# Performance work log

Hardware: AMD Instinct MI355X
Metric: run time of the kernel (lower is better)

## Reference

```python
import jax, jax.numpy as jnp
import numpy as np

N, K, D_IN, D_OUT = 50000, 16, 128, 256
C1, C2 = D_OUT // 4, D_OUT // 2  # 64, 128
E = N * K


def _lin(key, din, dout):
    return jax.random.normal(key, (din, dout), jnp.float32) * 0.02


def setup_inputs() -> dict:
    key = jax.random.key(0)
    ks = jax.random.split(key, 16)
    x = jax.random.normal(ks[0], (N, D_IN), jnp.float32)
    pos = jax.random.normal(ks[1], (N, 3), jnp.float32)
    normals = jax.random.normal(ks[2], (N, 3), jnp.float32)
    batch = jnp.zeros((N,), jnp.int32)
    # fixed k-regular graph standing in for knn_graph(pos, K); src != dst so
    # darboux's sqrt(|pos_j-pos_i|^2) is smooth everywhere
    dst = jnp.repeat(jnp.arange(N, dtype=jnp.int32), K)            # [E]
    off = jax.random.randint(ks[3], (E,), 1, N, jnp.int32)
    src = (dst + off) % N                                          # [E]
    edge_index = jnp.stack([src, dst])                             # [2,E]
    inp = dict(x=x, pos=pos, batch=batch, normals=normals, edge_index=edge_index)

    def add_mlp(name, k, din, dout):
        inp[name + '_w'] = _lin(k, din, dout)
        inp[name + '_b'] = jnp.zeros((dout,), jnp.float32)
        inp[name + '_g'] = jnp.ones((dout,), jnp.float32)
        inp[name + '_bt'] = jnp.zeros((dout,), jnp.float32)

    add_mlp('mlp1', ks[4], D_IN, D_OUT // 8)
    add_mlp('sc', ks[5], D_IN, D_OUT)
    add_mlp('mlp2', ks[6], C2, D_OUT)
    add_mlp('enc1', ks[7], 8, C1 // 2)
    inp['att1_w'] = _lin(ks[8], C1, C1)
    add_mlp('post1', ks[9], C1, C1)
    add_mlp('enc2', ks[10], 8, C2 // 2)
    inp['att2_w'] = _lin(ks[11], C2, C2)
    add_mlp('post2', ks[12], C2, C2)
    return inp


def _bn(h, g, bt, eps=1e-6):
    # BatchNorm1d, training-mode batch statistics (biased variance)
    m = h.mean(0)
    v = jnp.mean((h - m) ** 2, axis=0)
    return (h - m) * jax.lax.rsqrt(v + eps) * g + bt


def _lrelu(h):
    return jnp.where(h >= 0, h, 0.2 * h)


def _smlp(h, w, b, g, bt, act=True):
    # SharedMLP layer: Linear -> BN(eps=1e-6) -> LeakyReLU(0.2) (act optional)
    h = _bn(h @ w + b, g, bt)
    return _lrelu(h) if act else h


def _darboux(pi, pj, ni, nj):
    eps = 1e-10
    d = pj - pi                                            # [E,3]
    dot = lambda a, b: jnp.sum(a * b, axis=1, keepdims=True)
    nrm = lambda a: jnp.sqrt(jnp.sum(a * a, axis=1, keepdims=True))
    dist = nrm(d)
    lni, lnj = nrm(ni), nrm(nj)
    uq = jnp.cross(d, ni); vq = jnp.cross(uq, ni)
    uk = jnp.cross(d, nj); vk = jnp.cross(uk, nj)
    luq, lvq, luk, lvk = nrm(uq), nrm(vq), nrm(uk), nrm(vk)
    return jnp.concatenate([
        dist,
        dot(d, ni) / (dist * lni + eps),
        dot(d, nj) / (dist * lnj + eps),
        dot(ni, nj) / (lni * lnj + eps),
        dot(uq, uk) / (luq * luk + eps),
        dot(vq, vk) / (lvq * lvk + eps),
        dot(uq, vk) / (luq * lvk + eps),
        dot(vq, uk) / (lvq * luk + eps),
    ], axis=1)                                             # [E,8]


def _seg_softmax(h, idx, n):
    m = jax.ops.segment_max(h, idx, num_segments=n)        # [N,C]
    e = jnp.exp(h - m[idx])
    s = jax.ops.segment_sum(e, idx, num_segments=n)
    return e / (s[idx] + 1e-16)


def _lfa(src, dst, n, x, pos, normals, ew, eb, eg, ebt, aw, pw, pb, pg, pbt):
    rel = _darboux(pos[dst], pos[src], normals[dst], normals[src])  # [E,8]
    lse = _smlp(rel, ew, eb, eg, ebt)                               # [E,C/2]
    lf = jnp.concatenate([x[src], lse], axis=1)                     # [E,C]
    att = lf @ aw                                                   # [E,C]
    scores = _seg_softmax(att, dst, n)
    agg = jax.ops.segment_sum(scores * lf, dst, num_segments=n)     # [N,C]
    return _smlp(agg, pw, pb, pg, pbt)


def reference(x, pos, batch, normals, edge_index,
              mlp1_w, mlp1_b, mlp1_g, mlp1_bt,
              sc_w, sc_b, sc_g, sc_bt,
              mlp2_w, mlp2_b, mlp2_g, mlp2_bt,
              enc1_w, enc1_b, enc1_g, enc1_bt, att1_w,
              post1_w, post1_b, post1_g, post1_bt,
              enc2_w, enc2_b, enc2_g, enc2_bt, att2_w,
              post2_w, post2_b, post2_g, post2_bt):
    n = x.shape[0]
    src, dst = edge_index[0], edge_index[1]
    shortcut = _smlp(x, sc_w, sc_b, sc_g, sc_bt, act=False)         # [N,d_out]
    h = _smlp(x, mlp1_w, mlp1_b, mlp1_g, mlp1_bt)                   # [N,d_out//8]
    h = _lfa(src, dst, n, h, pos, normals,
             enc1_w, enc1_b, enc1_g, enc1_bt, att1_w,
             post1_w, post1_b, post1_g, post1_bt)                   # [N,d_out//4]
    h = _lfa(src, dst, n, h, pos, normals,
             enc2_w, enc2_b, enc2_g, enc2_bt, att2_w,
             post2_w, post2_b, post2_g, post2_bt)                   # [N,d_out//2]
    h = _smlp(h, mlp2_w, mlp2_b, mlp2_g, mlp2_bt, act=False)        # [N,d_out]
    return _lrelu(h + shortcut)
```

## Files before the change

kernel.cpp:

```cpp
#include <hip/hip_runtime.h>
#include <hip/hip_bf16.h>
#include <math.h>


typedef __attribute__((ext_vector_type(8))) short short8;
typedef __attribute__((ext_vector_type(4))) float floatx4;

#define NPART 16
#define PSTRIDE 4096

__device__ __forceinline__ float lrelu_f(float v) { return v >= 0.f ? v : 0.2f * v; }

__device__ __forceinline__ uint asu(float f) {
    union { float f; uint u; } c; c.f = f; return c.u;
}
__device__ __forceinline__ unsigned short f2bf(float f) {
    union { __hip_bfloat16 h; unsigned short u; } cv;
    cv.h = __float2bfloat16(f);
    return cv.u;
}
__device__ __forceinline__ unsigned short f2bf_r(float f) {
    return (unsigned short)((asu(f) + 0x8000u) >> 16);
}
__device__ __forceinline__ uint pack2bf_r(float lo, float hi) {
// ... 12 lines not shown
{
    int gid = blockIdx.x * 256 + threadIdx.x;
    int base = 0;
    for (int s = 0; s < 7; s++) {
        int c = pa.seg[s].cnt;
        if (gid < base + c) {
            int fi = gid - base;
            const float* w = pa.seg[s].src;
            const int Cout = pa.seg[s].Cout, KK = pa.seg[s].KK;
            const int l15 = fi & 15, g = (fi >> 4) & 3, rest = fi >> 6;
            const int kk = rest % KK, nt = rest / KK;
            const int col = nt * 16 + l15;
            short8 v;
#pragma unroll
            for (int e = 0; e < 8; e++)
                v[e] = (short)f2bf(w[(size_t)(kk * 32 + g * 8 + e) * Cout + col]);
            *reinterpret_cast<short8*>(pa.seg[s].dst + (size_t)fi * 8) = v;
            return;
        }
        base += c;
    }
}

template<bool AFF, bool IN16, bool MLP1>
__global__ __launch_bounds__(256)
void lin_mfma_kernel(const void* __restrict__ inv, const float* __restrict__ aff,
                     const short* __restrict__ wp, const float* __restrict__ b,
                     unsigned short* __restrict__ out16, double* __restrict__ st,
                     const short* __restrict__ wp1, const float* __restrict__ b1,
                     unsigned short* __restrict__ out1, double* __restrict__ st1, int n)
{
    __shared__ __align__(16) char aS[64 * 256];
    const int tid = threadIdx.x;
    const int w = tid >> 6, grp = (tid >> 4) & 3, l15 = tid & 15, lane = tid & 63;
    const int row0 = blockIdx.x * 64;
    const int poff = (blockIdx.x & (NPART - 1)) * PSTRIDE;
    double* stp = st + poff;
    {
        const int r = tid >> 2;
        const int p = tid & 3;
        const int chbase = p * 32;
        const int gr = row0 + r;
        if (gr < n) {
#pragma unroll
            for (int u = 0; u < 4; u++) {
                float h[8];
                if constexpr (IN16) {
                    const unsigned short* hrow = (const unsigned short*)inv + (size_t)gr * 128 + chbase + u * 8;
                    uint4 raw = *reinterpret_cast<const uint4*>(hrow);
                    h[0] = bf2f((unsigned short)(raw.x & 0xFFFF)); h[1] = bf2f((unsigned short)(raw.x >> 16));
                    h[2] = bf2f((unsigned short)(raw.y & 0xFFFF)); h[3] = bf2f((unsigned short)(raw.y >> 16));
                    h[4] = bf2f((unsigned short)(raw.z & 0xFFFF)); h[5] = bf2f((unsigned short)(raw.z >> 16));
                    h[6] = bf2f((unsigned short)(raw.w & 0xFFFF)); h[7] = bf2f((unsigned short)(raw.w >> 16));
                } else {
                    const float* hrow = (const float*)inv + (size_t)gr * 128 + chbase + u * 8;
                    float4 h0 = *reinterpret_cast<const float4*>(hrow);
                    float4 h1 = *reinterpret_cast<const float4*>(hrow + 4);
                    h[0] = h0.x; h[1] = h0.y; h[2] = h0.z; h[3] = h0.w;
                    h[4] = h1.x; h[5] = h1.y; h[6] = h1.z; h[7] = h1.w;
                }
                if constexpr (AFF) {
                    const float* ar = aff + chbase + u * 8;
                    const float* cr = aff + 128 + chbase + u * 8;
#pragma unroll
                    for (int i2 = 0; i2 < 8; i2++)
                        h[i2] = lrelu_f(fmaf(h[i2], ar[i2], cr[i2]));
                }
                uint4 pk;
                pk.x = pack2bf_r(h[0], h[1]); pk.y = pack2bf_r(h[2], h[3]);
                pk.z = pack2bf_r(h[4], h[5]); pk.w = pack2bf_r(h[6], h[7]);
                const int unit = (chbase >> 3) + u;
                *reinterpret_cast<uint4*>(aS + r * 256 + ((unit ^ (r & 7)) << 4)) = pk;
            }
        }
    }
    __syncthreads();

    short8 B[4][4]; float bias[4];
#pragma unroll
    for (int t = 0; t < 4; t++) {
        const int nt = w * 4 + t;
        bias[t] = b[nt * 16 + l15];
#pragma unroll
        for (int kk = 0; kk < 4; kk++)
            B[t][kk] = *reinterpret_cast<const short8*>(wp + (size_t)(((nt * 4 + kk) * 4 + grp) * 16 + l15) * 8);
    }
    float ssum[4] = {0.f, 0.f, 0.f, 0.f}, ssq[4] = {0.f, 0.f, 0.f, 0.f};
#pragma unroll
    for (int mt = 0; mt < 4; mt++) {
        short8 a[4];
        const int arow = mt * 16 + l15;
#pragma unroll
        for (int kk = 0; kk < 4; kk++)
            a[kk] = *reinterpret_cast<const short8*>(aS + arow * 256 + ((((kk << 2) + grp) ^ (arow & 7)) << 4));
#pragma unroll
        for (int t = 0; t < 4; t++) {
            floatx4 acc = {bias[t], bias[t], bias[t], bias[t]};
#pragma unroll
            for (int kk = 0; kk < 4; kk++)
                acc = __builtin_amdgcn_mfma_f32_16x16x32_bf16(a[kk], B[t][kk], acc, 0, 0, 0);
            const int c = (w * 4 + t) * 16 + l15;
#pragma unroll
            for (int r = 0; r < 4; r++) {
                const int grow = row0 + mt * 16 + grp * 4 + r;
                if (grow < n) {
                    out16[(size_t)grow * 256 + c] = f2bf_r(acc[r]);
                    ssum[t] += acc[r];
                    ssq[t] = fmaf(acc[r], acc[r], ssq[t]);
                }
            }
        }
    }
#pragma unroll
    for (int t = 0; t < 4; t++) {
        float s = ssum[t], q = ssq[t];
        s += __shfl_xor(s, 16); s += __shfl_xor(s, 32);
        q += __shfl_xor(q, 16); q += __shfl_xor(q, 32);
        if (lane < 16) {
            const int c = (w * 4 + t) * 16 + l15;
            atomicAdd(&stp[c], (double)s);
            atomicAdd(&stp[256 + c], (double)q);
        }
    }

    if constexpr (MLP1) {
        if (w < 2) {
            double* stp1 = st1 + poff;
            const float bias1 = b1[w * 16 + l15];
            short8 B1[4];
#pragma unroll
            for (int kk = 0; kk < 4; kk++)
                B1[kk] = *reinterpret_cast<const short8*>(wp1 + (size_t)(((w * 4 + kk) * 4 + grp) * 16 + l15) * 8);
            float s1 = 0.f, q1 = 0.f;
#pragma unroll
            for (int mt = 0; mt < 4; mt++) {
                short8 a[4];
                const int arow = mt * 16 + l15;
#pragma unroll
                for (int kk = 0; kk < 4; kk++)
                    a[kk] = *reinterpret_cast<const short8*>(aS + arow * 256 + ((((kk << 2) + grp) ^ (arow & 7)) << 4));
                floatx4 acc = {bias1, bias1, bias1, bias1};
#pragma unroll
                for (int kk = 0; kk < 4; kk++)
                    acc = __builtin_amdgcn_mfma_f32_16x16x32_bf16(a[kk], B1[kk], acc, 0, 0, 0);
                const int c = w * 16 + l15;
#pragma unroll
                for (int r = 0; r < 4; r++) {
                    const int grow = row0 + mt * 16 + grp * 4 + r;
                    if (grow < n) {
                        out1[(size_t)grow * 32 + c] = f2bf_r(acc[r]);
                        s1 += acc[r];
                        q1 = fmaf(acc[r], acc[r], q1);
                    }
                }
            }
            s1 += __shfl_xor(s1, 16); s1 += __shfl_xor(s1, 32);
            q1 += __shfl_xor(q1, 16); q1 += __shfl_xor(q1, 32);
            if (lane < 16) {
                const int c = w * 16 + l15;
                atomicAdd(&stp1[c], (double)s1);
                atomicAdd(&stp1[32 + c], (double)q1);
            }
        }
    }
}

__global__ __launch_bounds__(256)
void edge_enc_kernel(const int* __restrict__ src, const float* __restrict__ pos,
                     const float* __restrict__ nrm, unsigned short* __restrict__ rel16,
                     int E, double* __restrict__ stM)
{
    float s8[8] = {0, 0, 0, 0, 0, 0, 0, 0};
    float M[36];
#pragma unroll
    for (int k = 0; k < 36; k++) M[k] = 0.f;
    const int tid = threadIdx.x;

    for (int e = blockIdx.x * 256 + tid; e < E; e += gridDim.x * 256) {
        const int d = e >> 4;
        const int s = src[e];
        const float pix = pos[3 * d], piy = pos[3 * d + 1], piz = pos[3 * d + 2];
        const float pjx = pos[3 * s], pjy = pos[3 * s + 1], pjz = pos[3 * s + 2];
        const float nix = nrm[3 * d], niy = nrm[3 * d + 1], niz = nrm[3 * d + 2];
        const float njx = nrm[3 * s], njy = nrm[3 * s + 1], njz = nrm[3 * s + 2];
        const float dx = pjx - pix, dy = pjy - piy, dz = pjz - piz;
        const float dist = sqrtf(dx * dx + dy * dy + dz * dz);
        const float lni = sqrtf(nix * nix + niy * niy + niz * niz);
        const float lnj = sqrtf(njx * njx + njy * njy + njz * njz);
        const float uqx = dy * niz - dz * niy, uqy = dz * nix - dx * niz, uqz = dx * niy - dy * nix;
        const float vqx = uqy * niz - uqz * niy, vqy = uqz * nix - uqx * niz, vqz = uqx * niy - uqy * nix;
        const float ukx = dy * njz - dz * njy, uky = dz * njx - dx * njz, ukz = dx * njy - dy * njx;
        const float vkx = uky * njz - ukz * njy, vky = ukz * njx - ukx * njz, vkz = ukx * njy - uky * njx;
        const float luq = sqrtf(uqx * uqx + uqy * uqy + uqz * uqz);
        const float lvq = sqrtf(vqx * vqx + vqy * vqy + vqz * vqz);
        const float luk = sqrtf(ukx * ukx + uky * uky + ukz * ukz);
        const float lvk = sqrtf(vkx * vkx + vky * vky + vkz * vkz);
        const float eps = 1e-10f;
        float rv[8];
        rv[0] = dist;
        rv[1] = (dx * nix + dy * niy + dz * niz) / (dist * lni + eps);
        rv[2] = (dx * njx + dy * njy + dz * njz) / (dist * lnj + eps);
        rv[3] = (nix * njx + niy * njy + niz * njz) / (lni * lnj + eps);
        rv[4] = (uqx * ukx + uqy * uky + uqz * ukz) / (luq * luk + eps);
        rv[5] = (vqx * vkx + vqy * vky + vqz * vkz) / (lvq * lvk + eps);
        rv[6] = (uqx * vkx + uqy * vky + uqz * vkz) / (luq * lvk + eps);
        rv[7] = (vqx * ukx + vqy * uky + vqz * ukz) / (lvq * luk + eps);
        uint4 pk;
        pk.x = pack2bf_r(rv[0], rv[1]); pk.y = pack2bf_r(rv[2], rv[3]);
        pk.z = pack2bf_r(rv[4], rv[5]); pk.w = pack2bf_r(rv[6], rv[7]);
        *reinterpret_cast<uint4*>(rel16 + (size_t)e * 8) = pk;
#pragma unroll
        for (int i = 0; i < 8; i++) s8[i] += rv[i];
#pragma unroll
        for (int i = 0; i < 8; i++)
#pragma unroll
            for (int j = i; j < 8; j++)
                M[i * 8 - (i * (i - 1)) / 2 + (j - i)] = fmaf(rv[i], rv[j], M[i * 8 - (i * (i - 1)) / 2 + (j - i)]);
    }
#pragma unroll
    for (int k = 0; k < 8; k++) {
        float v = s8[k];
        v += __shfl_xor(v, 1); v += __shfl_xor(v, 2); v += __shfl_xor(v, 4);
        v += __shfl_xor(v, 8); v += __shfl_xor(v, 16); v += __shfl_xor(v, 32);
        s8[k] = v;
    }
#pragma unroll
    for (int k = 0; k < 36; k++) {
        float v = M[k];
        v += __shfl_xor(v, 1); v += __shfl_xor(v, 2); v += __shfl_xor(v, 4);
        v += __shfl_xor(v, 8); v += __shfl_xor(v, 16); v += __shfl_xor(v, 32);
        M[k] = v;
    }
    __shared__ float red[4][44];
    const int w = tid >> 6, lane = tid & 63;
    if (lane == 0) {
#pragma unroll
        for (int k = 0; k < 8; k++) red[w][k] = s8[k];
#pragma unroll
        for (int k = 0; k < 36; k++) red[w][8 + k] = M[k];
    }
    __syncthreads();
    if (tid < 44) {
        float tot = red[0][tid] + red[1][tid] + red[2][tid] + red[3][tid];
        atomicAdd(&stM[(blockIdx.x & (NPART - 1)) * PSTRIDE + tid], (double)tot);
    }
}

__global__ void enc_finalize_kernel(const double* __restrict__ stM,
    const float* __restrict__ ew1, const float* __restrict__ eb1,
    const float* __restrict__ g1, const float* __restrict__ bt1, float* __restrict__ ac1,
    const float* __restrict__ ew2, const float* __restrict__ eb2,
    const float* __restrict__ g2, const float* __restrict__ bt2, float* __restrict__ ac2,
    float Ef)
{
    __shared__ double SM[44];
    const int tid = threadIdx.x;
    if (tid < 44) {
        double a = 0;
        for (int p = 0; p < NPART; p++) a += stM[p * PSTRIDE + tid];
        SM[tid] = a;
    }
    __syncthreads();
    if (tid < 96) {
        const bool is2 = tid < 64;
        const int c = is2 ? tid : tid - 64;
        const int HCc = is2 ? 64 : 32;
        const float* ew = is2 ? ew2 : ew1;
// ... 3 lines not shown
        for (int j = 0; j < 8; j++) wv[j] = ew[j * HCc + c];
        double dot = 0.0, quad = 0.0;
#pragma unroll
        for (int i = 0; i < 8; i++) {
            dot += SM[i] * (double)wv[i];
#pragma unroll
            for (int j = i; j < 8; j++) {
                const double mij = SM[8 + i * 8 - (i * (i - 1)) / 2 + (j - i)];
                quad += mij * (double)wv[i] * (double)wv[j] * ((i == j) ? 1.0 : 2.0);
            }
        }
        const double sum   = dot + (double)Ef * b;
        const double sumsq = quad + 2.0 * b * dot + (double)Ef * b * b;
        const double m = sum / Ef;
        const double v = sumsq / Ef - m * m;
        const float rstd = (float)(1.0 / sqrt(v + 1e-6));
        const float a = rstd * (is2 ? g2 : g1)[c];
        float* ac = is2 ? ac2 : ac1;
        ac[c] = a;
        ac[HCc + c] = fmaf(-(float)m, a, (is2 ? bt2 : bt1)[c]);
    }
}

struct FinSeg { const double* st; const float* g; const float* bt; float* ac; int C; float cnt; };
struct FinArgs { FinSeg seg[3]; };

__global__ void finalize_multi_kernel(FinArgs fa)
{
    FinSeg s = fa.seg[blockIdx.x];
    int c = threadIdx.x;
    if (c < s.C) {
        double sm = 0.0, sq = 0.0;
#pragma unroll
        for (int p = 0; p < NPART; p++) {
            sm += s.st[p * PSTRIDE + c];
            sq += s.st[p * PSTRIDE + s.C + c];
        }
        double m = sm / (double)s.cnt;
        double v = sq / (double)s.cnt - m * m;
        float rstd = (float)(1.0 / sqrt(v + 1e-6));
        float a = rstd * s.g[c];
        s.ac[c] = a;
        s.ac[s.C + c] = fmaf(-(float)m, a, s.bt[c]);
    }
}

template<int C>
__global__ void bnconv_kernel(const unsigned short* __restrict__ hv, const float* __restrict__ ac,
                              unsigned short* __restrict__ o, size_t total8)
{
    size_t i = (size_t)blockIdx.x * blockDim.x + threadIdx.x;
    size_t stride = (size_t)gridDim.x * blockDim.x;
    for (; i < total8; i += stride) {
        const size_t b = i * 8;
        const int c = (int)(b & (size_t)(C - 1));
        uint4 raw = *reinterpret_cast<const uint4*>(hv + b);
        float h[8];
        h[0] = bf2f((unsigned short)(raw.x & 0xFFFF)); h[1] = bf2f((unsigned short)(raw.x >> 16));
        h[2] = bf2f((unsigned short)(raw.y & 0xFFFF)); h[3] = bf2f((unsigned short)(raw.y >> 16));
        h[4] = bf2f((unsigned short)(raw.z & 0xFFFF)); h[5] = bf2f((unsigned short)(raw.z >> 16));
        h[6] = bf2f((unsigned short)(raw.w & 0xFFFF)); h[7] = bf2f((unsigned short)(raw.w >> 16));
        const float* ar = ac + c;
        const float* cr = ac + C + c;
        uint4 pk;
        pk.x = pack2bf_r(lrelu_f(fmaf(h[0], ar[0], cr[0])), lrelu_f(fmaf(h[1], ar[1], cr[1])));
        pk.y = pack2bf_r(lrelu_f(fmaf(h[2], ar[2], cr[2])), lrelu_f(fmaf(h[3], ar[3], cr[3])));
        pk.z = pack2bf_r(lrelu_f(fmaf(h[4], ar[4], cr[4])), lrelu_f(fmaf(h[5], ar[5], cr[5])));
        pk.w = pack2bf_r(lrelu_f(fmaf(h[6], ar[6], cr[6])), lrelu_f(fmaf(h[7], ar[7], cr[7])));
        *reinterpret_cast<uint4*>(o + b) = pk;
    }
}

template<int C, int NODES>
__global__ __launch_bounds__(256)
void lfa13_kernel(const unsigned short* __restrict__ hbn,
                  const unsigned short* __restrict__ rel16,
                  const int* __restrict__ src,
                  const float* __restrict__ ew, const float* __restrict__ eb,
                  const float* __restrict__ encac,
                  const short* __restrict__ attp, const short* __restrict__ postp,
                  const float* __restrict__ postb,
                  unsigned short* __restrict__ out16, double* __restrict__ st, int n)
{
    constexpr int HC = C / 2, NT = C / 16, NTW = NT / 4, KK = C / 32, ROWB = 2 * C;
    constexpr int ROWS = NODES * 16;
    constexpr int TPR = 256 / ROWS;
    constexpr int NTE = HC / 16;
    constexpr int NCOMB = (NODES * NTE) / 4;
    constexpr int NSTEP = 4 / NTE;

    __shared__ __align__(16) char lfS[ROWS * ROWB];
    __shared__ __align__(16) char aggS[16 * ROWB];
// ... 146 lines not shown
        const int c = (w * NTW + t) * 16 + l15;
        float s = 0.f, q = 0.f;
#pragma unroll
        for (int r = 0; r < 4; r++) {
            const int nb = grp * 4 + r;
            if (nb < NODES && node0 + nb < n) {
                const float v = accP[t][r] + pb[t];
                out16[(size_t)(node0 + nb) * C + c] = f2bf_r(v);
                s += v;
                q = fmaf(v, v, q);
            }
        }
        s += __shfl_xor(s, 16); s += __shfl_xor(s, 32);
        q += __shfl_xor(q, 16); q += __shfl_xor(q, 32);
        if (lane < 16) {
            atomicAdd(&stp[c], (double)s);
            atomicAdd(&stp[C + c], (double)q);
        }
    }
}

__global__ void final_kernel(float* __restrict__ out, const unsigned short* __restrict__ m2,
                             const unsigned short* __restrict__ xs,
                             const float* __restrict__ ac2, const float* __restrict__ acs,
                             int total4)
{
    int i = blockIdx.x * 256 + threadIdx.x;
    const int stride = gridDim.x * 256;
    for (; i < total4; i += stride) {
        ushort4 mv = reinterpret_cast<const ushort4*>(m2)[i];
        ushort4 xv = reinterpret_cast<const ushort4*>(xs)[i];
        const int c = (i & 63) << 2;
        float4 a2 = *reinterpret_cast<const float4*>(ac2 + c);
        float4 b2 = *reinterpret_cast<const float4*>(ac2 + 256 + c);
        float4 as = *reinterpret_cast<const float4*>(acs + c);
        float4 bs = *reinterpret_cast<const float4*>(acs + 256 + c);
        float4 v;
        v.x = lrelu_f(fmaf(bf2f(mv.x), a2.x, b2.x) + fmaf(bf2f(xv.x), as.x, bs.x));
        v.y = lrelu_f(fmaf(bf2f(mv.y), a2.y, b2.y) + fmaf(bf2f(xv.y), as.y, bs.y));
        v.z = lrelu_f(fmaf(bf2f(mv.z), a2.z, b2.z) + fmaf(bf2f(xv.z), as.z, bs.z));
        v.w = lrelu_f(fmaf(bf2f(mv.w), a2.w, b2.w) + fmaf(bf2f(xv.w), as.w, bs.w));
        reinterpret_cast<float4*>(out)[i] = v;
    }
}

extern "C" void kernel_launch(void* const* d_in, const int* in_sizes, int n_in,
                              void* d_out, int out_size, void* d_ws, size_t ws_size,
                              hipStream_t stream)
{
    const float* x       = (const float*)d_in[0];
    const float* pos     = (const float*)d_in[1];
    const float* normals = (const float*)d_in[3];
    const int*   eidx    = (const int*)d_in[4];

    const float* mlp1_w = (const float*)d_in[5];
    const float* mlp1_b = (const float*)d_in[6];
    const float* mlp1_g = (const float*)d_in[7];
    const float* mlp1_bt= (const float*)d_in[8];
    const float* sc_w   = (const float*)d_in[9];
    const float* sc_b   = (const float*)d_in[10];
    const float* sc_g   = (const float*)d_in[11];
    const float* sc_bt  = (const float*)d_in[12];
    const float* mlp2_w = (const float*)d_in[13];
    const float* mlp2_b = (const float*)d_in[14];
// ... 26 lines not shown

    char* base = (char*)d_ws;
    double* stats  = (double*)base;
    float*  affine = (float*)(base + 524288);
    short*  wprep  = (short*)(base + 540672);
    unsigned short* rel16 = (unsigned short*)(base + 786432);
    unsigned short* xs16  = rel16 + (size_t)E * 8;
    unsigned short* m2pre = xs16 + (size_t)n * 256;
    unsigned short* h1raw = m2pre + (size_t)n * 256;
    unsigned short* h1bn  = h1raw + (size_t)n * 32;
    unsigned short* hA16  = h1bn + (size_t)n * 32;
    unsigned short* hAbn  = hA16 + (size_t)n * 64;
    unsigned short* hB16  = hAbn + (size_t)n * 64;

    short* att1p = wprep;
    short* post1p = wprep + 4096;
    short* att2p = wprep + 8192;
    short* post2p = wprep + 24576;
    short* scp   = wprep + 40960;
    short* mlp2p = wprep + 73728;
    short* mlp1p = wprep + 106496;

    const int OF_MLP1 = 0, OF_ENCM = 64, OF_POST1 = 128, OF_POST2 = 512, OF_SC = 768, OF_MLP2 = 1280;
    const int AF_MLP1 = 0, AF_ENC1 = 64, AF_POST1 = 128, AF_ENC2 = 256,
              AF_POST2 = 512, AF_SC = 768, AF_MLP2 = 1280;

    hipMemsetAsync(stats, 0, NPART * 32768, stream);

    PrepArgs pa;
    pa.seg[0] = {att1_w,  att1p,  512,  64,  2};
    pa.seg[1] = {post1_w, post1p, 512,  64,  2};
    pa.seg[2] = {att2_w,  att2p,  2048, 128, 4};
    pa.seg[3] = {post2_w, post2p, 2048, 128, 4};
    pa.seg[4] = {sc_w,    scp,    4096, 256, 4};
    pa.seg[5] = {mlp2_w,  mlp2p,  4096, 256, 4};
    pa.seg[6] = {mlp1_w,  mlp1p,  512,  32,  4};
    wprep_kernel<<<54, 256, 0, stream>>>(pa);

    lin_mfma_kernel<false, false, true><<<(n + 63) / 64, 256, 0, stream>>>(
        x, nullptr, scp, sc_b, xs16, stats + OF_SC,
        mlp1p, mlp1_b, h1raw, stats + OF_MLP1, n);

    edge_enc_kernel<<<512, 256, 0, stream>>>(srcArr, pos, normals, rel16, E, stats + OF_ENCM);

    FinArgs f1;
    f1.seg[0] = {stats + OF_MLP1, mlp1_g, mlp1_bt, affine + AF_MLP1, 32, (float)n};
    f1.seg[1] = f1.seg[0]; f1.seg[2] = f1.seg[0];
    finalize_multi_kernel<<<1, 256, 0, stream>>>(f1);
    enc_finalize_kernel<<<1, 128, 0, stream>>>(stats + OF_ENCM,
        enc1_w, enc1_b, enc1_g, enc1_bt, affine + AF_ENC1,
        enc2_w, enc2_b, enc2_g, enc2_bt, affine + AF_ENC2, (float)E);

    bnconv_kernel<32><<<1024, 256, 0, stream>>>(h1raw, affine + AF_MLP1, h1bn, (size_t)n * 32 / 8);

    lfa13_kernel<64, 16><<<(n + 15) / 16, 256, 0, stream>>>(h1bn, rel16, srcArr, enc1_w, enc1_b,
        affine + AF_ENC1, att1p, post1p, post1_b, hA16, stats + OF_POST1, n);
    FinArgs f2;
    f2.seg[0] = {stats + OF_POST1, post1_g, post1_bt, affine + AF_POST1, 64, (float)n};
    f2.seg[1] = f2.seg[0]; f2.seg[2] = f2.seg[0];
    finalize_multi_kernel<<<1, 256, 0, stream>>>(f2);

    bnconv_kernel<64><<<1024, 256, 0, stream>>>(hA16, affine + AF_POST1, hAbn, (size_t)n * 64 / 8);

    lfa13_kernel<128, 8><<<(n + 7) / 8, 256, 0, stream>>>(hAbn, rel16, srcArr, enc2_w, enc2_b,
        affine + AF_ENC2, att2p, post2p, post2_b, hB16, stats + OF_POST2, n);
    FinArgs f3;
    f3.seg[0] = {stats + OF_POST2, post2_g, post2_bt, affine + AF_POST2, 128, (float)n};
    f3.seg[1] = f3.seg[0]; f3.seg[2] = f3.seg[0];
    finalize_multi_kernel<<<1, 256, 0, stream>>>(f3);

    lin_mfma_kernel<true, true, false><<<(n + 63) / 64, 256, 0, stream>>>(
        hB16, affine + AF_POST2, mlp2p, mlp2_b, m2pre, stats + OF_MLP2,
        nullptr, nullptr, nullptr, nullptr, n);
    FinArgs f4;
    f4.seg[0] = {stats + OF_MLP2, mlp2_g, mlp2_bt, affine + AF_MLP2, 256, (float)n};
    f4.seg[1] = {stats + OF_SC,   sc_g,   sc_bt,   affine + AF_SC,   256, (float)n};
    f4.seg[2] = f4.seg[0];
    finalize_multi_kernel<<<2, 256, 0, stream>>>(f4);

    final_kernel<<<2048, 256, 0, stream>>>(out, m2pre, xs16, affine + AF_MLP2, affine + AF_SC, n * 64);
}
```

Measured before the change: 237.0 us.

## Merge front linear and edge encoding into one launch; fold BN finalize into consumers

Combines the shortcut/mlp1 MFMA linear and the edge Darboux encoding into one kernel, with blocks split by index, so both run concurrently in a single launch. Removes the separate finalize_multi kernels: each consumer (bnconv, mlp2, final) now reduces the partitioned statistics into BN scale and shift itself at block start. The aim is fewer launches and less serialization, at the cost of every block redundantly reducing the stats partitions. The final kernel's grid is also reduced.

```diff
diff --git a/kernel.cpp b/kernel.cpp
--- a/kernel.cpp
+++ b/kernel.cpp
@@ -58,115 +58,98 @@
     }
 }
 
-template<bool AFF, bool IN16, bool MLP1>
 __global__ __launch_bounds__(256)
-void lin_mfma_kernel(const void* __restrict__ inv, const float* __restrict__ aff,
-                     const short* __restrict__ wp, const float* __restrict__ b,
-                     unsigned short* __restrict__ out16, double* __restrict__ st,
-                     const short* __restrict__ wp1, const float* __restrict__ b1,
-                     unsigned short* __restrict__ out1, double* __restrict__ st1, int n)
+void front_kernel(const float* __restrict__ x,
+                  const short* __restrict__ scp, const float* __restrict__ sc_b,
+                  unsigned short* __restrict__ xs16, double* __restrict__ stSC,
+                  const short* __restrict__ mlp1p, const float* __restrict__ mlp1_b,
+                  unsigned short* __restrict__ h1raw, double* __restrict__ stM1,
+                  const int* __restrict__ src, const float* __restrict__ pos,
+                  const float* __restrict__ nrm, unsigned short* __restrict__ rel16,
+                  double* __restrict__ stM, int n, int E, int nbFront)
 {
-    __shared__ __align__(16) char aS[64 * 256];
+    __shared__ __align__(16) char sbuf[16384];
     const int tid = threadIdx.x;
-    const int w = tid >> 6, grp = (tid >> 4) & 3, l15 = tid & 15, lane = tid & 63;
-    const int row0 = blockIdx.x * 64;
-    const int poff = (blockIdx.x & (NPART - 1)) * PSTRIDE;
-    double* stp = st + poff;
-    {
-        const int r = tid >> 2;
-        const int p = tid & 3;
-        const int chbase = p * 32;
-        const int gr = row0 + r;
-        if (gr < n) {
-#pragma unroll
-            for (int u = 0; u < 4; u++) {
-                float h[8];
-                if constexpr (IN16) {
-                    const unsigned short* hrow = (const unsigned short*)inv + (size_t)gr * 128 + chbase + u * 8;
-                    uint4 raw = *reinterpret_cast<const uint4*>(hrow);
-                    h[0] = bf2f((unsigned short)(raw.x & 0xFFFF)); h[1] = bf2f((unsigned short)(raw.x >> 16));
-                    h[2] = bf2f((unsigned short)(raw.y & 0xFFFF)); h[3] = bf2f((unsigned short)(raw.y >> 16));
-                    h[4] = bf2f((unsigned short)(raw.z & 0xFFFF)); h[5] = bf2f((unsigned short)(raw.z >> 16));
-                    h[6] = bf2f((unsigned short)(raw.w & 0xFFFF)); h[7] = bf2f((unsigned short)(raw.w >> 16));
-                } else {
-                    const float* hrow = (const float*)inv + (size_t)gr * 128 + chbase + u * 8;
-                    float4 h0 = *reinterpret_cast<const float4*>(hrow);
-                    float4 h1 = *reinterpret_cast<const float4*>(hrow + 4);
-                    h[0] = h0.x; h[1] = h0.y; h[2] = h0.z; h[3] = h0.w;
-                    h[4] = h1.x; h[5] = h1.y; h[6] = h1.z; h[7] = h1.w;
+
+    if ((int)blockIdx.x < nbFront) {
+        char* aS = sbuf;
+        const int w = tid >> 6, grp = (tid >> 4) & 3, l15 = tid & 15, lane = tid & 63;
+        const int row0 = blockIdx.x * 64;
+        const int poff = (blockIdx.x & (NPART - 1)) * PSTRIDE;
+        {
+            const int r = tid >> 2;
+            const int p = tid & 3;
+            const int chbase = p * 32;
+            const int gr = row0 + r;
+            if (gr < n) {
+                const float* hrow = x + (size_t)gr * 128 + chbase;
+#pragma unroll
+                for (int u = 0; u < 4; u++) {
+                    float4 h0 = *reinterpret_cast<const float4*>(hrow + u * 8);
+                    float4 h1 = *reinterpret_cast<const float4*>(hrow + u * 8 + 4);
+                    uint4 pk;
+                    pk.x = pack2bf_r(h0.x, h0.y); pk.y = pack2bf_r(h0.z, h0.w);
+                    pk.z = pack2bf_r(h1.x, h1.y); pk.w = pack2bf_r(h1.z, h1.w);
+                    const int unit = (chbase >> 3) + u;
+                    *reinterpret_cast<uint4*>(aS + r * 256 + ((unit ^ (r & 7)) << 4)) = pk;
                 }
-                if constexpr (AFF) {
-                    const float* ar = aff + chbase + u * 8;
-                    const float* cr = aff + 128 + chbase + u * 8;
-#pragma unroll
-                    for (int i2 = 0; i2 < 8; i2++)
-                        h[i2] = lrelu_f(fmaf(h[i2], ar[i2], cr[i2]));
+            }
+        }
+        __syncthreads();
+
+        short8 B[4][4]; float bias[4];
+#pragma unroll
+        for (int t = 0; t < 4; t++) {
+            const int nt = w * 4 + t;
+            bias[t] = sc_b[nt * 16 + l15];
+#pragma unroll
+            for (int kk = 0; kk < 4; kk++)
+                B[t][kk] = *reinterpret_cast<const short8*>(scp + (size_t)(((nt * 4 + kk) * 4 + grp) * 16 + l15) * 8);
+        }
+        float ssum[4] = {0.f, 0.f, 0.f, 0.f}, ssq[4] = {0.f, 0.f, 0.f, 0.f};
+#pragma unroll
+        for (int mt = 0; mt < 4; mt++) {
+            short8 a[4];
+            const int arow = mt * 16 + l15;
+#pragma unroll
+            for (int kk = 0; kk < 4; kk++)
+                a[kk] = *reinterpret_cast<const short8*>(aS + arow * 256 + ((((kk << 2) + grp) ^ (arow & 7)) << 4));
+#pragma unroll
+            for (int t = 0; t < 4; t++) {
+                floatx4 acc = {bias[t], bias[t], bias[t], bias[t]};
+#pragma unroll
+                for (int kk = 0; kk < 4; kk++)
+                    acc = __builtin_amdgcn_mfma_f32_16x16x32_bf16(a[kk], B[t][kk], acc, 0, 0, 0);
+                const int c = (w * 4 + t) * 16 + l15;
+#pragma unroll
+                for (int r = 0; r < 4; r++) {
+                    const int grow = row0 + mt * 16 + grp * 4 + r;
+                    if (grow < n) {
+                        xs16[(size_t)grow * 256 + c] = f2bf_r(acc[r]);
+                        ssum[t] += acc[r];
+                        ssq[t] = fmaf(acc[r], acc[r], ssq[t]);
+                    }
                 }
-                uint4 pk;
-                pk.x = pack2bf_r(h[0], h[1]); pk.y = pack2bf_r(h[2], h[3]);
-                pk.z = pack2bf_r(h[4], h[5]); pk.w = pack2bf_r(h[6], h[7]);
-                const int unit = (chbase >> 3) + u;
-                *reinterpret_cast<uint4*>(aS + r * 256 + ((unit ^ (r & 7)) << 4)) = pk;
-            }
-        }
-    }
-    __syncthreads();
-
-    short8 B[4][4]; float bias[4];
-#pragma unroll
-    for (int t = 0; t < 4; t++) {
-        const int nt = w * 4 + t;
-        bias[t] = b[nt * 16 + l15];
-#pragma unroll
-        for (int kk = 0; kk < 4; kk++)
-            B[t][kk] = *reinterpret_cast<const short8*>(wp + (size_t)(((nt * 4 + kk) * 4 + grp) * 16 + l15) * 8);
-    }
-    float ssum[4] = {0.f, 0.f, 0.f, 0.f}, ssq[4] = {0.f, 0.f, 0.f, 0.f};
-#pragma unroll
-    for (int mt = 0; mt < 4; mt++) {
-        short8 a[4];
-        const int arow = mt * 16 + l15;
-#pragma unroll
-        for (int kk = 0; kk < 4; kk++)
-            a[kk] = *reinterpret_cast<const short8*>(aS + arow * 256 + ((((kk << 2) + grp) ^ (arow & 7)) << 4));
+            }
+        }
 #pragma unroll
         for (int t = 0; t < 4; t++) {
-            floatx4 acc = {bias[t], bias[t], bias[t], bias[t]};
+            float s = ssum[t], q = ssq[t];
+            s += __shfl_xor(s, 16); s += __shfl_xor(s, 32);
+            q += __shfl_xor(q, 16); q += __shfl_xor(q, 32);
+            if (lane < 16) {
+                const int c = (w * 4 + t) * 16 + l15;
+                atomicAdd(&stSC[poff + c], (double)s);
+                atomicAdd(&stSC[poff + 256 + c], (double)q);
+            }
+        }
+
+        if (w < 2) {
+            const float bias1 = mlp1_b[w * 16 + l15];
+            short8 B1[4];
 #pragma unroll
             for (int kk = 0; kk < 4; kk++)
-                acc = __builtin_amdgcn_mfma_f32_16x16x32_bf16(a[kk], B[t][kk], acc, 0, 0, 0);
-            const int c = (w * 4 + t) * 16 + l15;
-#pragma unroll
-            for (int r = 0; r < 4; r++) {
-                const int grow = row0 + mt * 16 + grp * 4 + r;
-                if (grow < n) {
-                    out16[(size_t)grow * 256 + c] = f2bf_r(acc[r]);
-                    ssum[t] += acc[r];
-                    ssq[t] = fmaf(acc[r], acc[r], ssq[t]);
-                }
-            }
-        }
-    }
-#pragma unroll
-    for (int t = 0; t < 4; t++) {
-        float s = ssum[t], q = ssq[t];
-        s += __shfl_xor(s, 16); s += __shfl_xor(s, 32);
-        q += __shfl_xor(q, 16); q += __shfl_xor(q, 32);
-        if (lane < 16) {
-            const int c = (w * 4 + t) * 16 + l15;
-            atomicAdd(&stp[c], (double)s);
-            atomicAdd(&stp[256 + c], (double)q);
-        }
-    }
-
-    if constexpr (MLP1) {
-        if (w < 2) {
-            double* stp1 = st1 + poff;
-            const float bias1 = b1[w * 16 + l15];
-            short8 B1[4];
-#pragma unroll
-            for (int kk = 0; kk < 4; kk++)
-                B1[kk] = *reinterpret_cast<const short8*>(wp1 + (size_t)(((w * 4 + kk) * 4 + grp) * 16 + l15) * 8);
+                B1[kk] = *reinterpret_cast<const short8*>(mlp1p + (size_t)(((w * 4 + kk) * 4 + grp) * 16 + l15) * 8);
             float s1 = 0.f, q1 = 0.f;
 #pragma unroll
             for (int mt = 0; mt < 4; mt++) {
@@ -184,7 +167,7 @@
                 for (int r = 0; r < 4; r++) {
                     const int grow = row0 + mt * 16 + grp * 4 + r;
                     if (grow < n) {
-                        out1[(size_t)grow * 32 + c] = f2bf_r(acc[r]);
+                        h1raw[(size_t)grow * 32 + c] = f2bf_r(acc[r]);
                         s1 += acc[r];
                         q1 = fmaf(acc[r], acc[r], q1);
                     }
@@ -194,91 +177,86 @@
             q1 += __shfl_xor(q1, 16); q1 += __shfl_xor(q1, 32);
             if (lane < 16) {
                 const int c = w * 16 + l15;
-                atomicAdd(&stp1[c], (double)s1);
-                atomicAdd(&stp1[32 + c], (double)q1);
-            }
-        }
-    }
-}
-
-__global__ __launch_bounds__(256)
-void edge_enc_kernel(const int* __restrict__ src, const float* __restrict__ pos,
-                     const float* __restrict__ nrm, unsigned short* __restrict__ rel16,
-                     int E, double* __restrict__ stM)
-{
-    float s8[8] = {0, 0, 0, 0, 0, 0, 0, 0};
-    float M[36];
-#pragma unroll
-    for (int k = 0; k < 36; k++) M[k] = 0.f;
-    const int tid = threadIdx.x;
-
-    for (int e = blockIdx.x * 256 + tid; e < E; e += gridDim.x * 256) {
-        const int d = e >> 4;
-        const int s = src[e];
-        const float pix = pos[3 * d], piy = pos[3 * d + 1], piz = pos[3 * d + 2];
-        const float pjx = pos[3 * s], pjy = pos[3 * s + 1], pjz = pos[3 * s + 2];
-        const float nix = nrm[3 * d], niy = nrm[3 * d + 1], niz = nrm[3 * d + 2];
-        const float njx = nrm[3 * s], njy = nrm[3 * s + 1], njz = nrm[3 * s + 2];
-        const float dx = pjx - pix, dy = pjy - piy, dz = pjz - piz;
-        const float dist = sqrtf(dx * dx + dy * dy + dz * dz);
-        const float lni = sqrtf(nix * nix + niy * niy + niz * niz);
-        const float lnj = sqrtf(njx * njx + njy * njy + njz * njz);
-        const float uqx = dy * niz - dz * niy, uqy = dz * nix - dx * niz, uqz = dx * niy - dy * nix;
-        const float vqx = uqy * niz - uqz * niy, vqy = uqz * nix - uqx * niz, vqz = uqx * niy - uqy * nix;
-        const float ukx = dy * njz - dz * njy, uky = dz * njx - dx * njz, ukz = dx * njy - dy * njx;
-        const float vkx = uky * njz - ukz * njy, vky = ukz * njx - ukx * njz, vkz = ukx * njy - uky * njx;
-        const float luq = sqrtf(uqx * uqx + uqy * uqy + uqz * uqz);
-        const float lvq = sqrtf(vqx * vqx + vqy * vqy + vqz * vqz);
-        const float luk = sqrtf(ukx * ukx + uky * uky + ukz * ukz);
-        const float lvk = sqrtf(vkx * vkx + vky * vky + vkz * vkz);
-        const float eps = 1e-10f;
-        float rv[8];
-        rv[0] = dist;
-        rv[1] = (dx * nix + dy * niy + dz * niz) / (dist * lni + eps);
-        rv[2] = (dx * njx + dy * njy + dz * njz) / (dist * lnj + eps);
-        rv[3] = (nix * njx + niy * njy + niz * njz) / (lni * lnj + eps);
-        rv[4] = (uqx * ukx + uqy * uky + uqz * ukz) / (luq * luk + eps);
-        rv[5] = (vqx * vkx + vqy * vky + vqz * vkz) / (lvq * lvk + eps);
-        rv[6] = (uqx * vkx + uqy * vky + uqz * vkz) / (luq * lvk + eps);
-        rv[7] = (vqx * ukx + vqy * uky + vqz * ukz) / (lvq * luk + eps);
-        uint4 pk;
-        pk.x = pack2bf_r(rv[0], rv[1]); pk.y = pack2bf_r(rv[2], rv[3]);
-        pk.z = pack2bf_r(rv[4], rv[5]); pk.w = pack2bf_r(rv[6], rv[7]);
-        *reinterpret_cast<uint4*>(rel16 + (size_t)e * 8) = pk;
-#pragma unroll
-        for (int i = 0; i < 8; i++) s8[i] += rv[i];
-#pragma unroll
-        for (int i = 0; i < 8; i++)
-#pragma unroll
-            for (int j = i; j < 8; j++)
-                M[i * 8 - (i * (i - 1)) / 2 + (j - i)] = fmaf(rv[i], rv[j], M[i * 8 - (i * (i - 1)) / 2 + (j - i)]);
-    }
-#pragma unroll
-    for (int k = 0; k < 8; k++) {
-        float v = s8[k];
-        v += __shfl_xor(v, 1); v += __shfl_xor(v, 2); v += __shfl_xor(v, 4);
-        v += __shfl_xor(v, 8); v += __shfl_xor(v, 16); v += __shfl_xor(v, 32);
-        s8[k] = v;
-    }
-#pragma unroll
-    for (int k = 0; k < 36; k++) {
-        float v = M[k];
-        v += __shfl_xor(v, 1); v += __shfl_xor(v, 2); v += __shfl_xor(v, 4);
-        v += __shfl_xor(v, 8); v += __shfl_xor(v, 16); v += __shfl_xor(v, 32);
-        M[k] = v;
-    }
-    __shared__ float red[4][44];
-    const int w = tid >> 6, lane = tid & 63;
-    if (lane == 0) {
-#pragma unroll
-        for (int k = 0; k < 8; k++) red[w][k] = s8[k];
-#pragma unroll
-        for (int k = 0; k < 36; k++) red[w][8 + k] = M[k];
-    }
-    __syncthreads();
-    if (tid < 44) {
-        float tot = red[0][tid] + red[1][tid] + red[2][tid] + red[3][tid];
-        atomicAdd(&stM[(blockIdx.x & (NPART - 1)) * PSTRIDE + tid], (double)tot);
+                atomicAdd(&stM1[poff + c], (double)s1);
+                atomicAdd(&stM1[poff + 32 + c], (double)q1);
+            }
+        }
+    } else {
+        const int ebid = blockIdx.x - nbFront;
+        const int ngrid = gridDim.x - nbFront;
+        float s8[8] = {0, 0, 0, 0, 0, 0, 0, 0};
+        float M[36];
+#pragma unroll
+        for (int k = 0; k < 36; k++) M[k] = 0.f;
+
+        for (int e = ebid * 256 + tid; e < E; e += ngrid * 256) {
+            const int d = e >> 4;
+            const int s = src[e];
+            const float pix = pos[3 * d], piy = pos[3 * d + 1], piz = pos[3 * d + 2];
+            const float pjx = pos[3 * s], pjy = pos[3 * s + 1], pjz = pos[3 * s + 2];
+            const float nix = nrm[3 * d], niy = nrm[3 * d + 1], niz = nrm[3 * d + 2];
+            const float njx = nrm[3 * s], njy = nrm[3 * s + 1], njz = nrm[3 * s + 2];
+            const float dx = pjx - pix, dy = pjy - piy, dz = pjz - piz;
+            const float dist = sqrtf(dx * dx + dy * dy + dz * dz);
+            const float lni = sqrtf(nix * nix + niy * niy + niz * niz);
+            const float lnj = sqrtf(njx * njx + njy * njy + njz * njz);
+            const float uqx = dy * niz - dz * niy, uqy = dz * nix - dx * niz, uqz = dx * niy - dy * nix;
+            const float vqx = uqy * niz - uqz * niy, vqy = uqz * nix - uqx * niz, vqz = uqx * niy - uqy * nix;
+            const float ukx = dy * njz - dz * njy, uky = dz * njx - dx * njz, ukz = dx * njy - dy * njx;
+            const float vkx = uky * njz - ukz * njy, vky = ukz * njx - ukx * njz, vkz = ukx * njy - uky * njx;
+            const float luq = sqrtf(uqx * uqx + uqy * uqy + uqz * uqz);
+            const float lvq = sqrtf(vqx * vqx + vqy * vqy + vqz * vqz);
+            const float luk = sqrtf(ukx * ukx + uky * uky + ukz * ukz);
+            const float lvk = sqrtf(vkx * vkx + vky * vky + vkz * vkz);
+            const float eps = 1e-10f;
+            float rv[8];
+            rv[0] = dist;
+            rv[1] = (dx * nix + dy * niy + dz * niz) / (dist * lni + eps);
+            rv[2] = (dx * njx + dy * njy + dz * njz) / (dist * lnj + eps);
+            rv[3] = (nix * njx + niy * njy + niz * njz) / (lni * lnj + eps);
+            rv[4] = (uqx * ukx + uqy * uky + uqz * ukz) / (luq * luk + eps);
+            rv[5] = (vqx * vkx + vqy * vky + vqz * vkz) / (lvq * lvk + eps);
+            rv[6] = (uqx * vkx + uqy * vky + uqz * vkz) / (luq * lvk + eps);
+            rv[7] = (vqx * ukx + vqy * uky + vqz * ukz) / (lvq * luk + eps);
+            uint4 pk;
+            pk.x = pack2bf_r(rv[0], rv[1]); pk.y = pack2bf_r(rv[2], rv[3]);
+            pk.z = pack2bf_r(rv[4], rv[5]); pk.w = pack2bf_r(rv[6], rv[7]);
+            *reinterpret_cast<uint4*>(rel16 + (size_t)e * 8) = pk;
+#pragma unroll
+            for (int i = 0; i < 8; i++) s8[i] += rv[i];
+#pragma unroll
+            for (int i = 0; i < 8; i++)
+#pragma unroll
+                for (int j = i; j < 8; j++)
+                    M[i * 8 - (i * (i - 1)) / 2 + (j - i)] = fmaf(rv[i], rv[j], M[i * 8 - (i * (i - 1)) / 2 + (j - i)]);
+        }
+#pragma unroll
+        for (int k = 0; k < 8; k++) {
+            float v = s8[k];
+            v += __shfl_xor(v, 1); v += __shfl_xor(v, 2); v += __shfl_xor(v, 4);
+            v += __shfl_xor(v, 8); v += __shfl_xor(v, 16); v += __shfl_xor(v, 32);
+            s8[k] = v;
+        }
+#pragma unroll
+        for (int k = 0; k < 36; k++) {
+            float v = M[k];
+            v += __shfl_xor(v, 1); v += __shfl_xor(v, 2); v += __shfl_xor(v, 4);
+            v += __shfl_xor(v, 8); v += __shfl_xor(v, 16); v += __shfl_xor(v, 32);
+            M[k] = v;
+        }
+        float (*red)[44] = reinterpret_cast<float (*)[44]>(sbuf);
+        const int w = tid >> 6, lane = tid & 63;
+        if (lane == 0) {
+#pragma unroll
+            for (int k = 0; k < 8; k++) red[w][k] = s8[k];
+#pragma unroll
+            for (int k = 0; k < 36; k++) red[w][8 + k] = M[k];
+        }
+        __syncthreads();
+        if (tid < 44) {
+            float tot = red[0][tid] + red[1][tid] + red[2][tid] + red[3][tid];
+            atomicAdd(&stM[(ebid & (NPART - 1)) * PSTRIDE + tid], (double)tot);
+        }
     }
 }
 
@@ -328,34 +306,30 @@
     }
 }
 
-struct FinSeg { const double* st; const float* g; const float* bt; float* ac; int C; float cnt; };
-struct FinArgs { FinSeg seg[3]; };
-
-__global__ void finalize_multi_kernel(FinArgs fa)
+template<int C>
+__global__ void bnconv_fin_kernel(const unsigned short* __restrict__ hv,
+                                  const double* __restrict__ st,
+                                  const float* __restrict__ g, const float* __restrict__ bt,
+                                  float cnt, unsigned short* __restrict__ o, size_t total8)
 {
-    FinSeg s = fa.seg[blockIdx.x];
-    int c = threadIdx.x;
-    if (c < s.C) {
+    __shared__ float acS[2 * C];
+    const int tid = threadIdx.x;
+    if (tid < C) {
         double sm = 0.0, sq = 0.0;
 #pragma unroll
         for (int p = 0; p < NPART; p++) {
-            sm += s.st[p * PSTRIDE + c];
-            sq += s.st[p * PSTRIDE + s.C + c];
-        }
-        double m = sm / (double)s.cnt;
-        double v = sq / (double)s.cnt - m * m;
+            sm += st[p * PSTRIDE + tid];
+            sq += st[p * PSTRIDE + C + tid];
+        }
+        double m = sm / (double)cnt;
+        double v = sq / (double)cnt - m * m;
         float rstd = (float)(1.0 / sqrt(v + 1e-6));
-        float a = rstd * s.g[c];
-        s.ac[c] = a;
-        s.ac[s.C + c] = fmaf(-(float)m, a, s.bt[c]);
-    }
-}
-
-template<int C>
-__global__ void bnconv_kernel(const unsigned short* __restrict__ hv, const float* __restrict__ ac,
-                              unsigned short* __restrict__ o, size_t total8)
-{
-    size_t i = (size_t)blockIdx.x * blockDim.x + threadIdx.x;
+        float a = rstd * g[tid];
+        acS[tid] = a;
+        acS[C + tid] = fmaf(-(float)m, a, bt[tid]);
+    }
+    __syncthreads();
+    size_t i = (size_t)blockIdx.x * blockDim.x + tid;
     size_t stride = (size_t)gridDim.x * blockDim.x;
     for (; i < total8; i += stride) {
         const size_t b = i * 8;
@@ -366,14 +340,117 @@
         h[2] = bf2f((unsigned short)(raw.y & 0xFFFF)); h[3] = bf2f((unsigned short)(raw.y >> 16));
         h[4] = bf2f((unsigned short)(raw.z & 0xFFFF)); h[5] = bf2f((unsigned short)(raw.z >> 16));
         h[6] = bf2f((unsigned short)(raw.w & 0xFFFF)); h[7] = bf2f((unsigned short)(raw.w >> 16));
-        const float* ar = ac + c;
-        const float* cr = ac + C + c;
         uint4 pk;
-        pk.x = pack2bf_r(lrelu_f(fmaf(h[0], ar[0], cr[0])), lrelu_f(fmaf(h[1], ar[1], cr[1])));
-        pk.y = pack2bf_r(lrelu_f(fmaf(h[2], ar[2], cr[2])), lrelu_f(fmaf(h[3], ar[3], cr[3])));
-        pk.z = pack2bf_r(lrelu_f(fmaf(h[4], ar[4], cr[4])), lrelu_f(fmaf(h[5], ar[5], cr[5])));
-        pk.w = pack2bf_r(lrelu_f(fmaf(h[6], ar[6], cr[6])), lrelu_f(fmaf(h[7], ar[7], cr[7])));
+        pk.x = pack2bf_r(lrelu_f(fmaf(h[0], acS[c + 0], acS[C + c + 0])), lrelu_f(fmaf(h[1], acS[c + 1], acS[C + c + 1])));
+        pk.y = pack2bf_r(lrelu_f(fmaf(h[2], acS[c + 2], acS[C + c + 2])), lrelu_f(fmaf(h[3], acS[c + 3], acS[C + c + 3])));
+        pk.z = pack2bf_r(lrelu_f(fmaf(h[4], acS[c + 4], acS[C + c + 4])), lrelu_f(fmaf(h[5], acS[c + 5], acS[C + c + 5])));
+        pk.w = pack2bf_r(lrelu_f(fmaf(h[6], acS[c + 6], acS[C + c + 6])), lrelu_f(fmaf(h[7], acS[c + 7], acS[C + c + 7])));
         *reinterpret_cast<uint4*>(o + b) = pk;
+    }
+}
+
+__global__ __launch_bounds__(256)
+void mlp2_kernel(const unsigned short* __restrict__ inv,
+                 const double* __restrict__ staff, const float* __restrict__ ga,
+                 const float* __restrict__ bta, float cnt,
+                 const short* __restrict__ wp, const float* __restrict__ b,
+                 unsigned short* __restrict__ out16, double* __restrict__ st, int n)
+{
+    __shared__ __align__(16) char aS[64 * 256];
+    __shared__ float affS[256];
+    const int tid = threadIdx.x;
+    const int w = tid >> 6, grp = (tid >> 4) & 3, l15 = tid & 15, lane = tid & 63;
+    const int row0 = blockIdx.x * 64;
+    double* stp = st + (blockIdx.x & (NPART - 1)) * PSTRIDE;
+    if (tid < 128) {
+        double sm = 0.0, sq = 0.0;
+#pragma unroll
+        for (int p = 0; p < NPART; p++) {
+            sm += staff[p * PSTRIDE + tid];
+            sq += staff[p * PSTRIDE + 128 + tid];
+        }
+        double m = sm / (double)cnt;
+        double v = sq / (double)cnt - m * m;
+        float rstd = (float)(1.0 / sqrt(v + 1e-6));
+        float a = rstd * ga[tid];
+        affS[tid] = a;
+        affS[128 + tid] = fmaf(-(float)m, a, bta[tid]);
+    }
+    __syncthreads();
+    {
+        const int r = tid >> 2;
+        const int p = tid & 3;
+        const int chbase = p * 32;
+        const int gr = row0 + r;
+        if (gr < n) {
+#pragma unroll
+            for (int u = 0; u < 4; u++) {
+                const unsigned short* hrow = inv + (size_t)gr * 128 + chbase + u * 8;
+                uint4 raw = *reinterpret_cast<const uint4*>(hrow);
+                float h[8];
+                h[0] = bf2f((unsigned short)(raw.x & 0xFFFF)); h[1] = bf2f((unsigned short)(raw.x >> 16));
+                h[2] = bf2f((unsigned short)(raw.y & 0xFFFF)); h[3] = bf2f((unsigned short)(raw.y >> 16));
+                h[4] = bf2f((unsigned short)(raw.z & 0xFFFF)); h[5] = bf2f((unsigned short)(raw.z >> 16));
+                h[6] = bf2f((unsigned short)(raw.w & 0xFFFF)); h[7] = bf2f((unsigned short)(raw.w >> 16));
+                const int cb = chbase + u * 8;
+#pragma unroll
+                for (int i2 = 0; i2 < 8; i2++)
+                    h[i2] = lrelu_f(fmaf(h[i2], affS[cb + i2], affS[128 + cb + i2]));
+                uint4 pk;
+                pk.x = pack2bf_r(h[0], h[1]); pk.y = pack2bf_r(h[2], h[3]);
+                pk.z = pack2bf_r(h[4], h[5]); pk.w = pack2bf_r(h[6], h[7]);
+                const int unit = (chbase >> 3) + u;
+                *reinterpret_cast<uint4*>(aS + r * 256 + ((unit ^ (r & 7)) << 4)) = pk;
+            }
+        }
+    }
+    __syncthreads();
+
+    short8 B[4][4]; float bias[4];
+#pragma unroll
+    for (int t = 0; t < 4; t++) {
+        const int nt = w * 4 + t;
+        bias[t] = b[nt * 16 + l15];
+#pragma unroll
+        for (int kk = 0; kk < 4; kk++)
+            B[t][kk] = *reinterpret_cast<const short8*>(wp + (size_t)(((nt * 4 + kk) * 4 + grp) * 16 + l15) * 8);
+    }
+    float ssum[4] = {0.f, 0.f, 0.f, 0.f}, ssq[4] = {0.f, 0.f, 0.f, 0.f};
+#pragma unroll
+    for (int mt = 0; mt < 4; mt++) {
+        short8 a[4];
+        const int arow = mt * 16 + l15;
+#pragma unroll
+        for (int kk = 0; kk < 4; kk++)
+            a[kk] = *reinterpret_cast<const short8*>(aS + arow * 256 + ((((kk << 2) + grp) ^ (arow & 7)) << 4));
+#pragma unroll
+        for (int t = 0; t < 4; t++) {
+            floatx4 acc = {bias[t], bias[t], bias[t], bias[t]};
+#pragma unroll
+            for (int kk = 0; kk < 4; kk++)
+                acc = __builtin_amdgcn_mfma_f32_16x16x32_bf16(a[kk], B[t][kk], acc, 0, 0, 0);
+            const int c = (w * 4 + t) * 16 + l15;
+#pragma unroll
+            for (int r = 0; r < 4; r++) {
+                const int grow = row0 + mt * 16 + grp * 4 + r;
+                if (grow < n) {
+                    out16[(size_t)grow * 256 + c] = f2bf_r(acc[r]);
+                    ssum[t] += acc[r];
+                    ssq[t] = fmaf(acc[r], acc[r], ssq[t]);
+                }
+            }
+        }
+    }
+#pragma unroll
+    for (int t = 0; t < 4; t++) {
+        float s = ssum[t], q = ssq[t];
+        s += __shfl_xor(s, 16); s += __shfl_xor(s, 32);
+        q += __shfl_xor(q, 16); q += __shfl_xor(q, 32);
+        if (lane < 16) {
+            const int c = (w * 4 + t) * 16 + l15;
+            atomicAdd(&stp[c], (double)s);
+            atomicAdd(&stp[256 + c], (double)q);
+        }
     }
 }
 
@@ -566,24 +643,51 @@
 
 __global__ void final_kernel(float* __restrict__ out, const unsigned short* __restrict__ m2,
                              const unsigned short* __restrict__ xs,
-                             const float* __restrict__ ac2, const float* __restrict__ acs,
-                             int total4)
+                             const double* __restrict__ st2, const float* __restrict__ g2,
+                             const float* __restrict__ bt2,
+                             const double* __restrict__ stS, const float* __restrict__ gS,
+                             const float* __restrict__ btS, float cnt, int total4)
 {
-    int i = blockIdx.x * 256 + threadIdx.x;
+    __shared__ float A2[256], B2[256], AS[256], BS[256];
+    const int tid = threadIdx.x;
+    {
+        double sm = 0.0, sq = 0.0;
+#pragma unroll
+        for (int p = 0; p < NPART; p++) {
+            sm += st2[p * PSTRIDE + tid];
+            sq += st2[p * PSTRIDE + 256 + tid];
+        }
+        double m = sm / (double)cnt;
+        double v = sq / (double)cnt - m * m;
+        float rstd = (float)(1.0 / sqrt(v + 1e-6));
+        float a = rstd * g2[tid];
+        A2[tid] = a;
+        B2[tid] = fmaf(-(float)m, a, bt2[tid]);
+        sm = 0.0; sq = 0.0;
+#pragma unroll
+        for (int p = 0; p < NPART; p++) {
+            sm += stS[p * PSTRIDE + tid];
+            sq += stS[p * PSTRIDE + 256 + tid];
+        }
+        m = sm / (double)cnt;
+        v = sq / (double)cnt - m * m;
+        rstd = (float)(1.0 / sqrt(v + 1e-6));
+        a = rstd * gS[tid];
+        AS[tid] = a;
+        BS[tid] = fmaf(-(float)m, a, btS[tid]);
+    }
+    __syncthreads();
+    int i = blockIdx.x * 256 + tid;
     const int stride = gridDim.x * 256;
     for (; i < total4; i += stride) {
         ushort4 mv = reinterpret_cast<const ushort4*>(m2)[i];
         ushort4 xv = reinterpret_cast<const ushort4*>(xs)[i];
         const int c = (i & 63) << 2;
-        float4 a2 = *reinterpret_cast<const float4*>(ac2 + c);
-        float4 b2 = *reinterpret_cast<const float4*>(ac2 + 256 + c);
-        float4 as = *reinterpret_cast<const float4*>(acs + c);
-        float4 bs = *reinterpret_cast<const float4*>(acs + 256 + c);
         float4 v;
-        v.x = lrelu_f(fmaf(bf2f(mv.x), a2.x, b2.x) + fmaf(bf2f(xv.x), as.x, bs.x));
-        v.y = lrelu_f(fmaf(bf2f(mv.y), a2.y, b2.y) + fmaf(bf2f(xv.y), as.y, bs.y));
-        v.z = lrelu_f(fmaf(bf2f(mv.z), a2.z, b2.z) + fmaf(bf2f(xv.z), as.z, bs.z));
-        v.w = lrelu_f(fmaf(bf2f(mv.w), a2.w, b2.w) + fmaf(bf2f(xv.w), as.w, bs.w));
+        v.x = lrelu_f(fmaf(bf2f(mv.x), A2[c + 0], B2[c + 0]) + fmaf(bf2f(xv.x), AS[c + 0], BS[c + 0]));
+        v.y = lrelu_f(fmaf(bf2f(mv.y), A2[c + 1], B2[c + 1]) + fmaf(bf2f(xv.y), AS[c + 1], BS[c + 1]));
+        v.z = lrelu_f(fmaf(bf2f(mv.z), A2[c + 2], B2[c + 2]) + fmaf(bf2f(xv.z), AS[c + 2], BS[c + 2]));
+        v.w = lrelu_f(fmaf(bf2f(mv.w), A2[c + 3], B2[c + 3]) + fmaf(bf2f(xv.w), AS[c + 3], BS[c + 3]));
         reinterpret_cast<float4*>(out)[i] = v;
     }
 }
@@ -656,8 +760,7 @@
     short* mlp1p = wprep + 106496;
 
     const int OF_MLP1 = 0, OF_ENCM = 64, OF_POST1 = 128, OF_POST2 = 512, OF_SC = 768, OF_MLP2 = 1280;
-    const int AF_MLP1 = 0, AF_ENC1 = 64, AF_POST1 = 128, AF_ENC2 = 256,
-              AF_POST2 = 512, AF_SC = 768, AF_MLP2 = 1280;
+    const int AF_ENC1 = 64, AF_ENC2 = 256;
 
     hipMemsetAsync(stats, 0, NPART * 32768, stream);
 
@@ -671,46 +774,32 @@
     pa.seg[6] = {mlp1_w,  mlp1p,  512,  32,  4};
     wprep_kernel<<<54, 256, 0, stream>>>(pa);
 
-    lin_mfma_kernel<false, false, true><<<(n + 63) / 64, 256, 0, stream>>>(
-        x, nullptr, scp, sc_b, xs16, stats + OF_SC,
-        mlp1p, mlp1_b, h1raw, stats + OF_MLP1, n);
-
-    edge_enc_kernel<<<512, 256, 0, stream>>>(srcArr, pos, normals, rel16, E, stats + OF_ENCM);
-
-    FinArgs f1;
-    f1.seg[0] = {stats + OF_MLP1, mlp1_g, mlp1_bt, affine + AF_MLP1, 32, (float)n};
-    f1.seg[1] = f1.seg[0]; f1.seg[2] = f1.seg[0];
-    finalize_multi_kernel<<<1, 256, 0, stream>>>(f1);
+    const int nbFront = (n + 63) / 64;
+    front_kernel<<<nbFront + 512, 256, 0, stream>>>(
+        x, scp, sc_b, xs16, stats + OF_SC, mlp1p, mlp1_b, h1raw, stats + OF_MLP1,
+        srcArr, pos, normals, rel16, stats + OF_ENCM, n, E, nbFront);
+
     enc_finalize_kernel<<<1, 128, 0, stream>>>(stats + OF_ENCM,
         enc1_w, enc1_b, enc1_g, enc1_bt, affine + AF_ENC1,
         enc2_w, enc2_b, enc2_g, enc2_bt, affine + AF_ENC2, (float)E);
 
-    bnconv_kernel<32><<<1024, 256, 0, stream>>>(h1raw, affine + AF_MLP1, h1bn, (size_t)n * 32 / 8);
+    bnconv_fin_kernel<32><<<1024, 256, 0, stream>>>(h1raw, stats + OF_MLP1,
+        mlp1_g, mlp1_bt, (float)n, h1bn, (size_t)n * 32 / 8);
 
     lfa13_kernel<64, 16><<<(n + 15) / 16, 256, 0, stream>>>(h1bn, rel16, srcArr, enc1_w, enc1_b,
         affine + AF_ENC1, att1p, post1p, post1_b, hA16, stats + OF_POST1, n);
-    FinArgs f2;
-    f2.seg[0] = {stats + OF_POST1, post1_g, post1_bt, affine + AF_POST1, 64, (float)n};
-    f2.seg[1] = f2.seg[0]; f2.seg[2] = f2.seg[0];
-    finalize_multi_kernel<<<1, 256, 0, stream>>>(f2);
-
-    bnconv_kernel<64><<<1024, 256, 0, stream>>>(hA16, affine + AF_POST1, hAbn, (size_t)n * 64 / 8);
+
+    bnconv_fin_kernel<64><<<1024, 256, 0, stream>>>(hA16, stats + OF_POST1,
+        post1_g, post1_bt, (float)n, hAbn, (size_t)n * 64 / 8);
 
     lfa13_kernel<128, 8><<<(n + 7) / 8, 256, 0, stream>>>(hAbn, rel16, srcArr, enc2_w, enc2_b,
         affine + AF_ENC2, att2p, post2p, post2_b, hB16, stats + OF_POST2, n);
-    FinArgs f3;
-    f3.seg[0] = {stats + OF_POST2, post2_g, post2_bt, affine + AF_POST2, 128, (float)n};
-    f3.seg[1] = f3.seg[0]; f3.seg[2] = f3.seg[0];
-    finalize_multi_kernel<<<1, 256, 0, stream>>>(f3);
-
-    lin_mfma_kernel<true, true, false><<<(n + 63) / 64, 256, 0, stream>>>(
-        hB16, affine + AF_POST2, mlp2p, mlp2_b, m2pre, stats + OF_MLP2,
-        nullptr, nullptr, nullptr, nullptr, n);
-    FinArgs f4;
-    f4.seg[0] = {stats + OF_MLP2, mlp2_g, mlp2_bt, affine + AF_MLP2, 256, (float)n};
-    f4.seg[1] = {stats + OF_SC,   sc_g,   sc_bt,   affine + AF_SC,   256, (float)n};
-    f4.seg[2] = f4.seg[0];
-    finalize_multi_kernel<<<2, 256, 0, stream>>>(f4);
-
-    final_kernel<<<2048, 256, 0, stream>>>(out, m2pre, xs16, affine + AF_MLP2, affine + AF_SC, n * 64);
-}
+
+    mlp2_kernel<<<(n + 63) / 64, 256, 0, stream>>>(
+        hB16, stats + OF_POST2, post2_g, post2_bt, (float)n,
+        mlp2p, mlp2_b, m2pre, stats + OF_MLP2, n);
+
+    final_kernel<<<1024, 256, 0, stream>>>(out, m2pre, xs16,
+        stats + OF_MLP2, mlp2_g, mlp2_bt,
+        stats + OF_SC, sc_g, sc_bt, (float)n, n * 64);
+}
```

After: 232.8 us, median of 2. About the same (-1.8%).
